# Kernel optimization log

Measured on AMD Instinct MI355X. Metric: run time of the kernel, lower is better.

## Reference

```python
import jax, jax.numpy as jnp
import numpy as np

L = 512          # angles_max_length
R_CA = 3.8       # C-alpha - C-alpha virtual bond length (AB model)


def _B_mat(a, b):
    # Rigid transform of the AB C-alpha model: rot(alpha) about z, rot(beta), translate R along x.
    ca, sa = jnp.cos(a), jnp.sin(a)
    cb, sb = jnp.cos(b), jnp.sin(b)
    z = jnp.zeros_like(a)
    o = jnp.ones_like(a)
    rows = [
        [ca, -sa * cb,  sa * sb, R_CA * ca],
        [sa,  ca * cb, -ca * sb, R_CA * sa],
        [z,   sb,       cb,      z],
        [z,   z,        z,       o],
    ]
    return jnp.stack([jnp.stack(r, -1) for r in rows], -2)  # (..., 4, 4)


def _dB_da(a, b):
    ca, sa = jnp.cos(a), jnp.sin(a)
    cb, sb = jnp.cos(b), jnp.sin(b)
    z = jnp.zeros_like(a)
    rows = [
        [-sa, -ca * cb,  ca * sb, -R_CA * sa],
        [ ca, -sa * cb,  sa * sb,  R_CA * ca],
        [z, z, z, z],
        [z, z, z, z],
    ]
    return jnp.stack([jnp.stack(r, -1) for r in rows], -2)


def _dB_db(a, b):
    ca, sa = jnp.cos(a), jnp.sin(a)
    cb, sb = jnp.cos(b), jnp.sin(b)
    z = jnp.zeros_like(a)
    rows = [
        [z,  sa * sb,  sa * cb, z],
        [z, -ca * sb, -ca * cb, z],
        [z,  cb,      -sb,      z],
        [z, z, z, z],
    ]
    return jnp.stack([jnp.stack(r, -1) for r in rows], -2)


def setup_inputs() -> dict:
    key = jax.random.key(0)
    k1, k2, k3 = jax.random.split(key, 3)
    input_angles = jax.random.normal(k1, (32, 2, L), dtype=jnp.float32)
    input_coords = jax.random.normal(k2, (32, 3 * (L + 1)), dtype=jnp.float32)
    angles_length = jax.random.randint(k3, (32,), 0, L, dtype=jnp.int32)
    return {"input_angles": input_angles, "input_coords": input_coords,
            "angles_length": angles_length}


def reference(input_angles, input_coords, angles_length):
    Bsz = input_angles.shape[0]
    alpha = input_angles[:, 0, :]  # (B, L)
    beta = input_angles[:, 1, :]

    Bm = _B_mat(alpha, beta)  # (B, L, 4, 4)
    # Prefix products M_i = B_0 @ ... @ B_i (order-preserving associative scan).
    M = jax.lax.associative_scan(lambda x, y: x @ y, Bm, axis=1)
    eye = jnp.broadcast_to(jnp.eye(4, dtype=Bm.dtype), (Bsz, 1, 4, 4))
    M_prev = jnp.concatenate([eye, M[:, :-1]], axis=1)  # M_{i-1}

    # Rigid-transform inverse of M_i: [R^T, -R^T t; 0 1]
    Rm = M[..., :3, :3]
    t = M[..., :3, 3:]
    Rt = jnp.swapaxes(Rm, -1, -2)
    bottom = jnp.broadcast_to(jnp.array([0., 0., 0., 1.], Bm.dtype), (Bsz, L, 1, 4))
    Minv = jnp.concatenate(
        [jnp.concatenate([Rt, -(Rt @ t)], axis=-1), bottom], axis=-2)

    # F_i^q = M_{i-1} dB_i/dq M_i^{-1};  dr_j/dq_i = F_i^q r_j^h  (for j > i)
    Fa = M_prev @ _dB_da(alpha, beta) @ Minv  # (B, L, 4, 4)
    Fb = M_prev @ _dB_db(alpha, beta) @ Minv

    coords = input_coords.reshape(Bsz, L + 1, 3)
    rh = jnp.concatenate([coords, jnp.ones((Bsz, L + 1, 1), coords.dtype)], -1)

    ga = jnp.einsum('blij,bmj->blmi', Fa, rh)[..., :3]  # (B, L, L+1, 3)
    gb = jnp.einsum('blij,bmj->blmi', Fb, rh)[..., :3]

    i = jnp.arange(L)[:, None]
    j = jnp.arange(L + 1)[None, :]
    lens = angles_length[:, None, None]
    mask = ((j > i) & (i < lens) & (j <= lens))[..., None]
    ga = jnp.where(mask, ga, 0.0)
    gb = jnp.where(mask, gb, 0.0)

    out = jnp.stack([ga, gb], axis=1)  # (B, 2, L, L+1, 3)
    return out.reshape(Bsz, 2, 3 * L * (L + 1))
```

## Files before the change

### kernel.cpp

```cpp
#include <hip/hip_runtime.h>

#define LSEQ 512
#define RCA 3.8f

struct Aff { float m[3][4]; };

__device__ __forceinline__ Aff compose(const Aff& A, const Aff& B) {
    Aff C;
#pragma unroll
    for (int i = 0; i < 3; ++i) {
#pragma unroll
        for (int j = 0; j < 4; ++j) {
            float v = A.m[i][0] * B.m[0][j] + A.m[i][1] * B.m[1][j] + A.m[i][2] * B.m[2][j];
            if (j == 3) v += A.m[i][3];
            C.m[i][j] = v;
        }
    }
    return C;
}

__device__ __forceinline__ Aff shflUp(const Aff& a, int d) {
    Aff r;
#pragma unroll
    for (int i = 0; i < 3; ++i)
#pragma unroll
        for (int j = 0; j < 4; ++j)
            r.m[i][j] = __shfl_up(a.m[i][j], d, 64);
    return r;
}

__device__ __forceinline__ Aff makeB(float ca, float sa, float cb, float sb) {
    Aff B;
    B.m[0][0] = ca;  B.m[0][1] = -sa * cb; B.m[0][2] =  sa * sb; B.m[0][3] = RCA * ca;
    B.m[1][0] = sa;  B.m[1][1] =  ca * cb; B.m[1][2] = -ca * sb; B.m[1][3] = RCA * sa;
    B.m[2][0] = 0.f; B.m[2][1] =  sb;      B.m[2][2] =  cb;      B.m[2][3] = 0.f;
    return B;
}

__global__ __launch_bounds__(64) void scan_kernel(const float* __restrict__ angles,
                                                  float* __restrict__ F) {
    const int b = blockIdx.x;
    const int lane = threadIdx.x;

    const float* ap = angles + (size_t)b * 1024 + lane * 8;
    float4 a0 = *reinterpret_cast<const float4*>(ap);
    float4 a1 = *reinterpret_cast<const float4*>(ap + 4);
    float4 b0 = *reinterpret_cast<const float4*>(ap + 512);
    float4 b1 = *reinterpret_cast<const float4*>(ap + 516);
    float av[8] = {a0.x, a0.y, a0.z, a0.w, a1.x, a1.y, a1.z, a1.w};
    float bv[8] = {b0.x, b0.y, b0.z, b0.w, b1.x, b1.y, b1.z, b1.w};

    float ca[8], sa[8], cb[8], sb[8];
#pragma unroll
    for (int e = 0; e < 8; ++e) {
        sincosf(av[e], &sa[e], &ca[e]);
        sincosf(bv[e], &sb[e], &cb[e]);
    }

    Aff P = makeB(ca[0], sa[0], cb[0], sb[0]);
#pragma unroll
    for (int e = 1; e < 8; ++e) P = compose(P, makeB(ca[e], sa[e], cb[e], sb[e]));

    Aff S = P;
#pragma unroll
    for (int d = 1; d < 64; d <<= 1) {
        Aff o = shflUp(S, d);
        if (lane >= d) S = compose(o, S);
    }
    Aff Mprev = shflUp(S, 1);
    if (lane == 0) {
#pragma unroll
        for (int i = 0; i < 3; ++i)
#pragma unroll
            for (int j = 0; j < 4; ++j)
                Mprev.m[i][j] = (i == j) ? 1.f : 0.f;
    }

#pragma unroll
    for (int e = 0; e < 8; ++e) {
        const int l = lane * 8 + e;
        Aff B = makeB(ca[e], sa[e], cb[e], sb[e]);
        Aff M = compose(Mprev, B);

        float Rt[3][3], ti[3];
#pragma unroll
        for (int i = 0; i < 3; ++i)
#pragma unroll
            for (int j = 0; j < 3; ++j) Rt[i][j] = M.m[j][i];
#pragma unroll
        for (int i = 0; i < 3; ++i)
            ti[i] = -(M.m[0][i] * M.m[0][3] + M.m[1][i] * M.m[1][3] + M.m[2][i] * M.m[2][3]);

        float d0[4] = {-sa[e], -ca[e] * cb[e],  ca[e] * sb[e], -RCA * sa[e]};
        float d1[4] = { ca[e], -sa[e] * cb[e],  sa[e] * sb[e],  RCA * ca[e]};
        float e01 =  sa[e] * sb[e], e02 =  sa[e] * cb[e];
        float e11 = -ca[e] * sb[e], e12 = -ca[e] * cb[e];
        float e21 =  cb[e],         e22 = -sb[e];

        float Ga[3][4], Gb[3][4];
#pragma unroll
        for (int i = 0; i < 3; ++i) {
            float p0 = Mprev.m[i][0], p1 = Mprev.m[i][1], p2 = Mprev.m[i][2];
#pragma unroll
            for (int j = 0; j < 4; ++j) Ga[i][j] = p0 * d0[j] + p1 * d1[j];
            Gb[i][0] = 0.f;
            Gb[i][1] = p0 * e01 + p1 * e11 + p2 * e21;
            Gb[i][2] = p0 * e02 + p1 * e12 + p2 * e22;
            Gb[i][3] = 0.f;
        }

        float W[24];
#pragma unroll
        for (int i = 0; i < 3; ++i) {
#pragma unroll
            for (int j = 0; j < 3; ++j) {
                W[i * 4 + j]      = Ga[i][0] * Rt[0][j] + Ga[i][1] * Rt[1][j] + Ga[i][2] * Rt[2][j];
                W[12 + i * 4 + j] = Gb[i][0] * Rt[0][j] + Gb[i][1] * Rt[1][j] + Gb[i][2] * Rt[2][j];
            }
            W[i * 4 + 3]      = Ga[i][0] * ti[0] + Ga[i][1] * ti[1] + Ga[i][2] * ti[2] + Ga[i][3];
            W[12 + i * 4 + 3] = Gb[i][0] * ti[0] + Gb[i][1] * ti[1] + Gb[i][2] * ti[2] + Gb[i][3];
        }

        float4* w4 = reinterpret_cast<float4*>(F + ((size_t)b * LSEQ + l) * 24);
        const float4* s4 = reinterpret_cast<const float4*>(W);
#pragma unroll
        for (int q = 0; q < 6; ++q) w4[q] = s4[q];

        Mprev = M;
    }
}

__global__ __launch_bounds__(256) void emit_kernel(const float* __restrict__ F,
                                                   const float* __restrict__ coords,
                                                   const int* __restrict__ lens,
                                                   float* __restrict__ out) {
    const int l = blockIdx.x;
    const int b = blockIdx.y;
    const int tid = threadIdx.x;

    __shared__ float sF[24];
    __shared__ float sC[1539];
    if (tid < 24) sF[tid] = F[((size_t)b * LSEQ + l) * 24 + tid];
    for (int i = tid; i < 1539; i += 256) sC[i] = coords[(size_t)b * 1539 + i];
    __syncthreads();

    const int len = lens[b];
    const bool rowActive = (l < len);
    const size_t baseA = ((size_t)(b * 2) * LSEQ + l) * 1539;
    const size_t baseB = baseA + (size_t)LSEQ * 1539;

    const float f00 = sF[0],  f01 = sF[1],  f02 = sF[2],  f03 = sF[3];
    const float f10 = sF[4],  f11 = sF[5],  f12 = sF[6],  f13 = sF[7];
    const float f20 = sF[8],  f21 = sF[9],  f22 = sF[10], f23 = sF[11];
    const float g00 = sF[12], g01 = sF[13], g02 = sF[14], g03 = sF[15];
    const float g10 = sF[16], g11 = sF[17], g12 = sF[18], g13 = sF[19];
    const float g20 = sF[20], g21 = sF[21], g22 = sF[22], g23 = sF[23];

    for (int m = tid; m < 513; m += 256) {
        const float x = sC[m * 3];
        const float y = sC[m * 3 + 1];
        const float z = sC[m * 3 + 2];
        const bool act = rowActive && (m > l) && (m <= len);
        const float s = act ? 1.f : 0.f;

        float3 va, vb;
        va.x = s * (f00 * x + f01 * y + f02 * z + f03);
        va.y = s * (f10 * x + f11 * y + f12 * z + f13);
        va.z = s * (f20 * x + f21 * y + f22 * z + f23);
        vb.x = s * (g00 * x + g01 * y + g02 * z + g03);
        vb.y = s * (g10 * x + g11 * y + g12 * z + g13);
        vb.z = s * (g20 * x + g21 * y + g22 * z + g23);

        *reinterpret_cast<float3*>(out + baseA + (size_t)m * 3) = va;
        *reinterpret_cast<float3*>(out + baseB + (size_t)m * 3) = vb;
    }
}

extern "C" void kernel_launch(void* const* d_in, const int* in_sizes, int n_in,
                              void* d_out, int out_size, void* d_ws, size_t ws_size,
                              hipStream_t stream) {
    const float* angles = (const float*)d_in[0];
    const float* coords = (const float*)d_in[1];
    const int*   lens   = (const int*)d_in[2];
    float* out = (float*)d_out;
    float* F = (float*)d_ws;

    scan_kernel<<<32, 64, 0, stream>>>(angles, F);
    emit_kernel<<<dim3(LSEQ, 32), 256, 0, stream>>>(F, coords, lens, out);
}
```

Measured before the change: 228.5 us.

## Parallelize scan across 512 threads and emit four rows per block

The scan kernel now uses 512 threads per batch, one per angle. Each wave does a shuffle scan, then the wave totals are combined serially through shared memory, replacing the old scheme of 8 serial elements per lane in a single wave. The emit kernel now handles four rows per block, keeps coordinates in registers read straight from global memory instead of staging them in shared memory, and launches a quarter as many blocks. This is meant to shorten the serial scan and cut per-block setup cost in the store-bound emit, at the price of more registers and a loop over wave totals whose length grows with the wave index.

```diff
diff --git a/kernel.cpp b/kernel.cpp
--- a/kernel.cpp
+++ b/kernel.cpp
@@ -37,142 +37,150 @@
     return B;
 }
 
-__global__ __launch_bounds__(64) void scan_kernel(const float* __restrict__ angles,
-                                                  float* __restrict__ F) {
+__global__ __launch_bounds__(512) void scan_kernel(const float* __restrict__ angles,
+                                                   float* __restrict__ F) {
     const int b = blockIdx.x;
-    const int lane = threadIdx.x;
+    const int tid = threadIdx.x;
+    const int lane = tid & 63;
+    const int w = tid >> 6;
 
-    const float* ap = angles + (size_t)b * 1024 + lane * 8;
-    float4 a0 = *reinterpret_cast<const float4*>(ap);
-    float4 a1 = *reinterpret_cast<const float4*>(ap + 4);
-    float4 b0 = *reinterpret_cast<const float4*>(ap + 512);
-    float4 b1 = *reinterpret_cast<const float4*>(ap + 516);
-    float av[8] = {a0.x, a0.y, a0.z, a0.w, a1.x, a1.y, a1.z, a1.w};
-    float bv[8] = {b0.x, b0.y, b0.z, b0.w, b1.x, b1.y, b1.z, b1.w};
+    __shared__ float sT[8][12];
 
-    float ca[8], sa[8], cb[8], sb[8];
-#pragma unroll
-    for (int e = 0; e < 8; ++e) {
-        sincosf(av[e], &sa[e], &ca[e]);
-        sincosf(bv[e], &sb[e], &cb[e]);
-    }
+    const float a  = angles[(size_t)b * 1024 + tid];
+    const float be = angles[(size_t)b * 1024 + 512 + tid];
+    float sa, ca, sb, cb;
+    sincosf(a, &sa, &ca);
+    sincosf(be, &sb, &cb);
 
-    Aff P = makeB(ca[0], sa[0], cb[0], sb[0]);
-#pragma unroll
-    for (int e = 1; e < 8; ++e) P = compose(P, makeB(ca[e], sa[e], cb[e], sb[e]));
-
-    Aff S = P;
+    Aff S = makeB(ca, sa, cb, sb);
 #pragma unroll
     for (int d = 1; d < 64; d <<= 1) {
         Aff o = shflUp(S, d);
         if (lane >= d) S = compose(o, S);
     }
-    Aff Mprev = shflUp(S, 1);
-    if (lane == 0) {
+
+    if (lane == 63) {
 #pragma unroll
-        for (int i = 0; i < 3; ++i)
+        for (int k = 0; k < 12; ++k) sT[w][k] = S.m[k / 4][k % 4];
+    }
+    __syncthreads();
+
+    Aff E;
 #pragma unroll
-            for (int j = 0; j < 4; ++j)
-                Mprev.m[i][j] = (i == j) ? 1.f : 0.f;
+    for (int i = 0; i < 3; ++i)
+#pragma unroll
+        for (int j = 0; j < 4; ++j) E.m[i][j] = (i == j) ? 1.f : 0.f;
+    for (int k = 0; k < w; ++k) {
+        Aff T;
+#pragma unroll
+        for (int q = 0; q < 12; ++q) T.m[q / 4][q % 4] = sT[k][q];
+        E = compose(E, T);
     }
 
+    const Aff Sp = shflUp(S, 1);
+    const Aff M = compose(E, S);
+    Aff Mprev;
+    if (lane == 0) Mprev = E;
+    else           Mprev = compose(E, Sp);
+
+    float Rt[3][3], ti[3];
 #pragma unroll
-    for (int e = 0; e < 8; ++e) {
-        const int l = lane * 8 + e;
-        Aff B = makeB(ca[e], sa[e], cb[e], sb[e]);
-        Aff M = compose(Mprev, B);
+    for (int i = 0; i < 3; ++i)
+#pragma unroll
+        for (int j = 0; j < 3; ++j) Rt[i][j] = M.m[j][i];
+#pragma unroll
+    for (int i = 0; i < 3; ++i)
+        ti[i] = -(M.m[0][i] * M.m[0][3] + M.m[1][i] * M.m[1][3] + M.m[2][i] * M.m[2][3]);
 
-        float Rt[3][3], ti[3];
+    float d0[4] = {-sa, -ca * cb,  ca * sb, -RCA * sa};
+    float d1[4] = { ca, -sa * cb,  sa * sb,  RCA * ca};
+    float e01 =  sa * sb, e02 =  sa * cb;
+    float e11 = -ca * sb, e12 = -ca * cb;
+    float e21 =  cb,      e22 = -sb;
+
+    float Ga[3][4], Gb[3][4];
 #pragma unroll
-        for (int i = 0; i < 3; ++i)
+    for (int i = 0; i < 3; ++i) {
+        float p0 = Mprev.m[i][0], p1 = Mprev.m[i][1], p2 = Mprev.m[i][2];
 #pragma unroll
-            for (int j = 0; j < 3; ++j) Rt[i][j] = M.m[j][i];
+        for (int j = 0; j < 4; ++j) Ga[i][j] = p0 * d0[j] + p1 * d1[j];
+        Gb[i][0] = 0.f;
+        Gb[i][1] = p0 * e01 + p1 * e11 + p2 * e21;
+        Gb[i][2] = p0 * e02 + p1 * e12 + p2 * e22;
+        Gb[i][3] = 0.f;
+    }
+
+    float W[24];
 #pragma unroll
-        for (int i = 0; i < 3; ++i)
-            ti[i] = -(M.m[0][i] * M.m[0][3] + M.m[1][i] * M.m[1][3] + M.m[2][i] * M.m[2][3]);
+    for (int i = 0; i < 3; ++i) {
+#pragma unroll
+        for (int j = 0; j < 3; ++j) {
+            W[i * 4 + j]      = Ga[i][0] * Rt[0][j] + Ga[i][1] * Rt[1][j] + Ga[i][2] * Rt[2][j];
+            W[12 + i * 4 + j] = Gb[i][0] * Rt[0][j] + Gb[i][1] * Rt[1][j] + Gb[i][2] * Rt[2][j];
+        }
+        W[i * 4 + 3]      = Ga[i][0] * ti[0] + Ga[i][1] * ti[1] + Ga[i][2] * ti[2] + Ga[i][3];
+        W[12 + i * 4 + 3] = Gb[i][0] * ti[0] + Gb[i][1] * ti[1] + Gb[i][2] * ti[2] + Gb[i][3];
+    }
 
-        float d0[4] = {-sa[e], -ca[e] * cb[e],  ca[e] * sb[e], -RCA * sa[e]};
-        float d1[4] = { ca[e], -sa[e] * cb[e],  sa[e] * sb[e],  RCA * ca[e]};
-        float e01 =  sa[e] * sb[e], e02 =  sa[e] * cb[e];
-        float e11 = -ca[e] * sb[e], e12 = -ca[e] * cb[e];
-        float e21 =  cb[e],         e22 = -sb[e];
-
-        float Ga[3][4], Gb[3][4];
+    float4* w4 = reinterpret_cast<float4*>(F + ((size_t)b * LSEQ + tid) * 24);
+    const float4* s4 = reinterpret_cast<const float4*>(W);
 #pragma unroll
-        for (int i = 0; i < 3; ++i) {
-            float p0 = Mprev.m[i][0], p1 = Mprev.m[i][1], p2 = Mprev.m[i][2];
-#pragma unroll
-            for (int j = 0; j < 4; ++j) Ga[i][j] = p0 * d0[j] + p1 * d1[j];
-            Gb[i][0] = 0.f;
-            Gb[i][1] = p0 * e01 + p1 * e11 + p2 * e21;
-            Gb[i][2] = p0 * e02 + p1 * e12 + p2 * e22;
-            Gb[i][3] = 0.f;
-        }
-
-        float W[24];
-#pragma unroll
-        for (int i = 0; i < 3; ++i) {
-#pragma unroll
-            for (int j = 0; j < 3; ++j) {
-                W[i * 4 + j]      = Ga[i][0] * Rt[0][j] + Ga[i][1] * Rt[1][j] + Ga[i][2] * Rt[2][j];
-                W[12 + i * 4 + j] = Gb[i][0] * Rt[0][j] + Gb[i][1] * Rt[1][j] + Gb[i][2] * Rt[2][j];
-            }
-            W[i * 4 + 3]      = Ga[i][0] * ti[0] + Ga[i][1] * ti[1] + Ga[i][2] * ti[2] + Ga[i][3];
-            W[12 + i * 4 + 3] = Gb[i][0] * ti[0] + Gb[i][1] * ti[1] + Gb[i][2] * ti[2] + Gb[i][3];
-        }
-
-        float4* w4 = reinterpret_cast<float4*>(F + ((size_t)b * LSEQ + l) * 24);
-        const float4* s4 = reinterpret_cast<const float4*>(W);
-#pragma unroll
-        for (int q = 0; q < 6; ++q) w4[q] = s4[q];
-
-        Mprev = M;
-    }
+    for (int q = 0; q < 6; ++q) w4[q] = s4[q];
 }
 
 __global__ __launch_bounds__(256) void emit_kernel(const float* __restrict__ F,
                                                    const float* __restrict__ coords,
                                                    const int* __restrict__ lens,
                                                    float* __restrict__ out) {
-    const int l = blockIdx.x;
     const int b = blockIdx.y;
+    const int l0 = blockIdx.x * 4;
     const int tid = threadIdx.x;
 
-    __shared__ float sF[24];
-    __shared__ float sC[1539];
-    if (tid < 24) sF[tid] = F[((size_t)b * LSEQ + l) * 24 + tid];
-    for (int i = tid; i < 1539; i += 256) sC[i] = coords[(size_t)b * 1539 + i];
+    __shared__ float sF[96];
+    if (tid < 96) sF[tid] = F[((size_t)b * LSEQ + l0) * 24 + tid];
     __syncthreads();
 
     const int len = lens[b];
-    const bool rowActive = (l < len);
-    const size_t baseA = ((size_t)(b * 2) * LSEQ + l) * 1539;
-    const size_t baseB = baseA + (size_t)LSEQ * 1539;
+    const float* cp = coords + (size_t)b * 1539;
 
-    const float f00 = sF[0],  f01 = sF[1],  f02 = sF[2],  f03 = sF[3];
-    const float f10 = sF[4],  f11 = sF[5],  f12 = sF[6],  f13 = sF[7];
-    const float f20 = sF[8],  f21 = sF[9],  f22 = sF[10], f23 = sF[11];
-    const float g00 = sF[12], g01 = sF[13], g02 = sF[14], g03 = sF[15];
-    const float g10 = sF[16], g11 = sF[17], g12 = sF[18], g13 = sF[19];
-    const float g20 = sF[20], g21 = sF[21], g22 = sF[22], g23 = sF[23];
+    const int m0 = tid, m1 = tid + 256, m2 = tid + 512;
+    const float cx0 = cp[m0 * 3], cy0 = cp[m0 * 3 + 1], cz0 = cp[m0 * 3 + 2];
+    const float cx1 = cp[m1 * 3], cy1 = cp[m1 * 3 + 1], cz1 = cp[m1 * 3 + 2];
+    const bool has2 = (m2 < 513);
+    float cx2 = 0.f, cy2 = 0.f, cz2 = 0.f;
+    if (has2) { cx2 = cp[m2 * 3]; cy2 = cp[m2 * 3 + 1]; cz2 = cp[m2 * 3 + 2]; }
 
-    for (int m = tid; m < 513; m += 256) {
-        const float x = sC[m * 3];
-        const float y = sC[m * 3 + 1];
-        const float z = sC[m * 3 + 2];
-        const bool act = rowActive && (m > l) && (m <= len);
-        const float s = act ? 1.f : 0.f;
+#pragma unroll
+    for (int i = 0; i < 4; ++i) {
+        const int l = l0 + i;
+        const float* f = sF + i * 24;
+        const float f00 = f[0],  f01 = f[1],  f02 = f[2],  f03 = f[3];
+        const float f10 = f[4],  f11 = f[5],  f12 = f[6],  f13 = f[7];
+        const float f20 = f[8],  f21 = f[9],  f22 = f[10], f23 = f[11];
+        const float g00 = f[12], g01 = f[13], g02 = f[14], g03 = f[15];
+        const float g10 = f[16], g11 = f[17], g12 = f[18], g13 = f[19];
+        const float g20 = f[20], g21 = f[21], g22 = f[22], g23 = f[23];
 
-        float3 va, vb;
-        va.x = s * (f00 * x + f01 * y + f02 * z + f03);
-        va.y = s * (f10 * x + f11 * y + f12 * z + f13);
-        va.z = s * (f20 * x + f21 * y + f22 * z + f23);
-        vb.x = s * (g00 * x + g01 * y + g02 * z + g03);
-        vb.y = s * (g10 * x + g11 * y + g12 * z + g13);
-        vb.z = s * (g20 * x + g21 * y + g22 * z + g23);
+        const size_t baseA = ((size_t)(b * 2) * LSEQ + l) * 1539;
+        const size_t baseB = baseA + (size_t)LSEQ * 1539;
+        const bool rowActive = (l < len);
 
-        *reinterpret_cast<float3*>(out + baseA + (size_t)m * 3) = va;
-        *reinterpret_cast<float3*>(out + baseB + (size_t)m * 3) = vb;
+        auto emit1 = [&](int m, float x, float y, float z) {
+            const float s = (rowActive && (m > l) && (m <= len)) ? 1.f : 0.f;
+            float3 va, vb;
+            va.x = s * (f00 * x + f01 * y + f02 * z + f03);
+            va.y = s * (f10 * x + f11 * y + f12 * z + f13);
+            va.z = s * (f20 * x + f21 * y + f22 * z + f23);
+            vb.x = s * (g00 * x + g01 * y + g02 * z + g03);
+            vb.y = s * (g10 * x + g11 * y + g12 * z + g13);
+            vb.z = s * (g20 * x + g21 * y + g22 * z + g23);
+            *reinterpret_cast<float3*>(out + baseA + (size_t)m * 3) = va;
+            *reinterpret_cast<float3*>(out + baseB + (size_t)m * 3) = vb;
+        };
+
+        emit1(m0, cx0, cy0, cz0);
+        emit1(m1, cx1, cy1, cz1);
+        if (has2) emit1(m2, cx2, cy2, cz2);
     }
 }
 
@@ -185,6 +193,6 @@
     float* out = (float*)d_out;
     float* F = (float*)d_ws;
 
-    scan_kernel<<<32, 64, 0, stream>>>(angles, F);
-    emit_kernel<<<dim3(LSEQ, 32), 256, 0, stream>>>(F, coords, lens, out);
+    scan_kernel<<<32, 512, 0, stream>>>(angles, F);
+    emit_kernel<<<dim3(128, 32), 256, 0, stream>>>(F, coords, lens, out);
 }
```

After: 206.4 us. 1.11x faster.
